# Performance work log

Hardware: AMD Instinct MI355X
Metric: run time of the kernel (lower is better)

Reference implementation:

```python
import jax, jax.numpy as jnp
import numpy as np
import math

Q, WAY, SHOT, M, D = 50, 5, 5, 196, 640
N_ITERS = 5
VAR_FLOOR = 0.01

def _inv_softplus(v):
    return math.log(math.expm1(v))

def setup_inputs() -> dict:
    key = jax.random.key(0)
    k1, k2, k3 = jax.random.split(key, 3)
    # L2-normalized tokens so cost = 1 - cosine sim is well-scaled
    q = jax.random.normal(k1, (Q, M, D), dtype=jnp.float32)
    q = q / jnp.linalg.norm(q, axis=-1, keepdims=True)
    s = jax.random.normal(k2, (WAY, SHOT, M, D), dtype=jnp.float32)
    s = s / jnp.linalg.norm(s, axis=-1, keepdims=True)
    var = jax.random.uniform(k3, (WAY, D), dtype=jnp.float32, minval=0.5, maxval=1.5)
    eps_raw = jnp.asarray(_inv_softplus(0.1), dtype=jnp.float32)           # eps_init=0.1
    tau_local_raw = jnp.asarray(_inv_softplus(1.0 - 0.01), dtype=jnp.float32)  # tau_local_init=1.0
    return {"query_tokens": q, "support_tokens": s, "variance": var,
            "eps_raw": eps_raw, "tau_local_raw": tau_local_raw}

def reference(query_tokens, support_tokens, variance, eps_raw, tau_local_raw):
    eps = jax.nn.softplus(eps_raw) + 1e-4
    tau = jax.nn.softplus(tau_local_raw) + 0.01
    way, shot, m, d = support_tokens.shape
    km = shot * m
    nq = query_tokens.shape[0]
    # dimension weights from variance (use_vhat_coupling=True)
    w = 1.0 / (variance + VAR_FLOOR)                              # [way, d]
    w = w / jnp.maximum(w.sum(axis=-1, keepdims=True), 1e-6) * d
    support_weighted = support_tokens.reshape(way, km, d) * w[:, None, :]
    sim = jnp.einsum('qmd,wkd->qwmk', query_tokens, support_weighted)  # [q, way, m, km]
    cost = 1.0 - sim
    log_K = -cost / eps
    log_mu = jnp.full((nq, way, m), -math.log(float(m)), dtype=log_K.dtype)
    log_nu = jnp.full((nq, way, km), -math.log(float(km)), dtype=log_K.dtype)

    def step(carry, _):
        u, v = carry
        v = log_nu - jax.nn.logsumexp(log_K + u[..., None], axis=-2)
        u = log_mu - jax.nn.logsumexp(log_K + v[..., None, :], axis=-1)
        return (u, v), None

    (u, v), _ = jax.lax.scan(step, (jnp.zeros_like(log_mu), jnp.zeros_like(log_nu)),
                             None, length=N_ITERS)
    gamma = jnp.exp(log_K + u[..., None] + v[..., None, :])
    ot_cost = jnp.sum(gamma * cost, axis=(-1, -2))                # [q, way]
    return -ot_cost / tau
```

## Files before the change

kernel.cpp:

```cpp
#include <hip/hip_runtime.h>
#include <hip/hip_bf16.h>
#include <hip/hip_fp16.h>

#define QN    50
#define NWAY  5
#define NPAIR 250
#define MM    196
#define KMM   980
#define DD    640
#define NITER 5

typedef __attribute__((ext_vector_type(8)))  short short8;
typedef __attribute__((ext_vector_type(16))) float f32x16;

#define EXP2F(x) __builtin_exp2f(x)
#define LOG2F(x) __builtin_log2f(x)
#define RCPF(x)  __builtin_amdgcn_rcpf(x)

__device__ __forceinline__ short bf16bits(float f) {
  __hip_bfloat16 h = __float2bfloat16(f);
  return *reinterpret_cast<short*>(&h);
}

__device__ __forceinline__ void h2AtomicAdd(__half2* addr, float a, float b) {
  unsigned int* ui = reinterpret_cast<unsigned int*>(addr);
  unsigned int old = __hip_atomic_load(ui, __ATOMIC_RELAXED, __HIP_MEMORY_SCOPE_AGENT);
  unsigned int assumed;
  do {
    assumed = old;
    __half2 cur = *reinterpret_cast<__half2*>(&assumed);
    float2 cf = __half22float2(cur);
    __half2 sum = __floats2half2_rn(cf.x + a, cf.y + b);
    unsigned int ns = *reinterpret_cast<unsigned int*>(&sum);
    old = atomicCAS(ui, assumed, ns);
  } while (old != assumed);
}

__global__ __launch_bounds__(256, 3)
void gemm_kernel(const float* __restrict__ qt, const float* __restrict__ st,
                 const float* __restrict__ var, const float* __restrict__ epsr,
                 __half* __restrict__ cost, __half* __restrict__ T1)
{
  __shared__ __align__(16) unsigned short Ash[128 * 64];
  __shared__ __align__(16) unsigned short Bsh[128 * 64];
  __shared__ __align__(16) float w_lds[DD];
  __shared__ float cs_lds[128];
  __shared__ float red_s;

  const int tid  = threadIdx.x;
  const int wv   = tid >> 6;
  const int lane = tid & 63;
  const int l31  = lane & 31;
  const int lh   = lane >> 5;
  const int wm   = wv >> 1;
  const int wn   = wv & 1;

  const int lg   = (blockIdx.x & 7) * 500 + (blockIdx.x >> 3);
  const int pair = lg >> 4;
  const int mt_  = (lg >> 3) & 1;
  const int nt_  = lg & 7;
  const int qi = pair / NWAY, wi = pair % NWAY;
  const int m0 = mt_ * 128, n0 = nt_ * 128;

  const float eps = logf(1.0f + expf(epsr[0])) + 1e-4f;
  const float C2  = 1.4426950408889634f / eps;

  float psum = 0.f;
  for (int d = tid; d < DD; d += 256) {
    float inv = 1.0f / (var[wi * DD + d] + 0.01f);
    w_lds[d] = inv; psum += inv;
  }
  #pragma unroll
  for (int s = 32; s; s >>= 1) psum += __shfl_xor(psum, s);
  if (tid == 0) red_s = 0.f;
  if (tid < 128) cs_lds[tid] = 0.f;
  __syncthreads();
  if (lane == 0) atomicAdd(&red_s, psum);
  __syncthreads();
  const float wsc = (float)DD / fmaxf(red_s, 1e-6f);
  for (int d = tid; d < DD; d += 256) w_lds[d] *= wsc;
  __syncthreads();

  const float* qb = qt + (size_t)qi * MM * DD;
  const float* sb = st + (size_t)wi * KMM * DD;

  f32x16 acc[2][2];
  #pragma unroll
  for (int i = 0; i < 2; ++i)
    #pragma unroll
    for (int j = 0; j < 2; ++j)
      #pragma unroll
      for (int e = 0; e < 16; ++e) acc[i][j][e] = 0.f;

  const int srow = tid >> 3;
  const int sslt = tid & 7;

  float4 ra0[4], ra1[4], rb0[4], rb1[4];

  #pragma unroll
  for (int i = 0; i < 4; ++i) {
    const int r = i * 32 + srow;
    const float* sa = qb + (size_t)min(m0 + r, MM - 1) * DD + sslt * 8;
    ra0[i] = *reinterpret_cast<const float4*>(sa);
    ra1[i] = *reinterpret_cast<const float4*>(sa + 4);
    const float* sbp = sb + (size_t)min(n0 + r, KMM - 1) * DD + sslt * 8;
    rb0[i] = *reinterpret_cast<const float4*>(sbp);
    rb1[i] = *reinterpret_cast<const float4*>(sbp + 4);
  }

  #pragma unroll
  for (int ks = 0; ks < 10; ++ks) {
    const int kd = ks * 64 + sslt * 8;
    float4 w0 = *reinterpret_cast<const float4*>(w_lds + kd);
    float4 w1 = *reinterpret_cast<const float4*>(w_lds + kd + 4);
    #pragma unroll
    for (int i = 0; i < 4; ++i) {
      const int r = i * 32 + srow;
      const int wslt = (sslt ^ (r & 7)) * 8;
      short8 pk;
      pk[0] = bf16bits(ra0[i].x); pk[1] = bf16bits(ra0[i].y);
      pk[2] = bf16bits(ra0[i].z); pk[3] = bf16bits(ra0[i].w);
      pk[4] = bf16bits(ra1[i].x); pk[5] = bf16bits(ra1[i].y);
      pk[6] = bf16bits(ra1[i].z); pk[7] = bf16bits(ra1[i].w);
      *reinterpret_cast<short8*>(&Ash[r * 64 + wslt]) = pk;
      short8 qk;
      qk[0] = bf16bits(rb0[i].x * w0.x); qk[1] = bf16bits(rb0[i].y * w0.y);
      qk[2] = bf16bits(rb0[i].z * w0.z); qk[3] = bf16bits(rb0[i].w * w0.w);
      qk[4] = bf16bits(rb1[i].x * w1.x); qk[5] = bf16bits(rb1[i].y * w1.y);
      qk[6] = bf16bits(rb1[i].z * w1.z); qk[7] = bf16bits(rb1[i].w * w1.w);
      *reinterpret_cast<short8*>(&Bsh[r * 64 + wslt]) = qk;
    }
    __syncthreads();
    if (ks < 9) {
      const int kn = (ks + 1) * 64 + sslt * 8;
      #pragma unroll
      for (int i = 0; i < 4; ++i) {
        const int r = i * 32 + srow;
        const float* sa = qb + (size_t)min(m0 + r, MM - 1) * DD + kn;
        ra0[i] = *reinterpret_cast<const float4*>(sa);
        ra1[i] = *reinterpret_cast<const float4*>(sa + 4);
        const float* sbp = sb + (size_t)min(n0 + r, KMM - 1) * DD + kn;
        rb0[i] = *reinterpret_cast<const float4*>(sbp);
        rb1[i] = *reinterpret_cast<const float4*>(sbp + 4);
      }
    }
    #pragma unroll
    for (int kk = 0; kk < 4; ++kk) {
      const int ph = ((kk * 2 + lh) ^ (l31 & 7)) * 8;
      short8 a0 = *reinterpret_cast<short8*>(&Ash[(wm * 64      + l31) * 64 + ph]);
      short8 a1 = *reinterpret_cast<short8*>(&Ash[(wm * 64 + 32 + l31) * 64 + ph]);
      short8 b0 = *reinterpret_cast<short8*>(&Bsh[(wn * 64      + l31) * 64 + ph]);
      short8 b1 = *reinterpret_cast<short8*>(&Bsh[(wn * 64 + 32 + l31) * 64 + ph]);
      acc[0][0] = __builtin_amdgcn_mfma_f32_32x32x16_bf16(a0, b0, acc[0][0], 0, 0, 0);
      acc[0][1] = __builtin_amdgcn_mfma_f32_32x32x16_bf16(a0, b1, acc[0][1], 0, 0, 0);
      acc[1][0] = __builtin_amdgcn_mfma_f32_32x32x16_bf16(a1, b0, acc[1][0], 0, 0, 0);
      acc[1][1] = __builtin_amdgcn_mfma_f32_32x32x16_bf16(a1, b1, acc[1][1], 0, 0, 0);
    }
    __syncthreads();
  }

  __half* cb = cost + (size_t)pair * MM * KMM;
  #pragma unroll
  for (int nt = 0; nt < 2; ++nt) {
    const int ncol = n0 + wn * 64 + nt * 32 + l31;
    float part = 0.f;
    #pragma unroll
    for (int mt = 0; mt < 2; ++mt) {
      #pragma unroll
      for (int r = 0; r < 16; ++r) {
        const int mrow = m0 + wm * 64 + mt * 32 + (r & 3) + 8 * (r >> 2) + 4 * lh;
        if (mrow < MM && ncol < KMM) {
          const float val = (acc[mt][nt][r] - 1.0f) * C2;
          cb[(size_t)mrow * KMM + ncol] = __float2half(val);
          part += EXP2F(val);
        }
      }
    }
    atomicAdd(&cs_lds[wn * 64 + nt * 32 + l31], part);
  }
  __syncthreads();
  if (tid < 64) {
    const int c0 = n0 + 2 * tid;
    if (c0 < KMM)
      h2AtomicAdd(reinterpret_cast<__half2*>(T1 + (size_t)pair * KMM + c0),
                  cs_lds[2 * tid], cs_lds[2 * tid + 1]);
  }
}

template<bool FIN>
__global__ __launch_bounds__(256)
void sweep_kernel(const __half* __restrict__ cost, const __half* __restrict__ Tin,
                  __half* __restrict__ Tout, const float* __restrict__ epsr,
                  const float* __restrict__ taur, float* __restrict__ outp)
{
  __shared__ float part[4][1024];
  const int tid  = threadIdx.x;
  const int wave = tid >> 6;
  const int lane = tid & 63;
  const int pair   = blockIdx.x / 7;
  const int mchunk = blockIdx.x % 7;

  const __half* cb = cost + (size_t)pair * MM * KMM;
  const __half* tp = Tin  + (size_t)pair * KMM;

  float iT[16], acc[16], p[16];
  #pragma unroll
  for (int j = 0; j < 4; ++j) {
    const int k = 4 * lane + 256 * j;
    if (k < KMM) {
      uint2 raw = *reinterpret_cast<const uint2*>(tp + k);
      float2 t01 = __half22float2(*reinterpret_cast<const __half2*>(&raw.x));
      float2 t23 = __half22float2(*reinterpret_cast<const __half2*>(&raw.y));
      iT[4 * j + 0] = RCPF(980.0f * t01.x);
      iT[4 * j + 1] = RCPF(980.0f * t01.y);
      iT[4 * j + 2] = RCPF(980.0f * t23.x);
      iT[4 * j + 3] = RCPF(980.0f * t23.y);
    } else {
      iT[4 * j + 0] = 0.f; iT[4 * j + 1] = 0.f;
      iT[4 * j + 2] = 0.f; iT[4 * j + 3] = 0.f;
    }
  }
  #pragma unroll
  for (int e = 0; e < 16; ++e) acc[e] = 0.f;

  float scal = 0.f, rowacc = 0.f;
  if (FIN) {
    const float eps = logf(1.0f + expf(epsr[0])) + 1e-4f;
    const float C2  = 1.4426950408889634f / eps;
    const float tau = logf(1.0f + expf(taur[0])) + 0.01f;
    scal = 1.0f / (tau * C2);
  }

  #pragma unroll
  for (int r = 0; r < 7; ++r) {
    const int m = mchunk * 28 + wave * 7 + r;
    const __half* rp = cb + (size_t)m * KMM;
    float A = 0.f, Bv = 0.f;
    #pragma unroll
    for (int j = 0; j < 4; ++j) {
      const int k = 4 * lane + 256 * j;
      if (k < KMM) {
        uint2 raw = *reinterpret_cast<const uint2*>(rp + k);
        float2 c01 = __half22float2(*reinterpret_cast<const __half2*>(&raw.x));
        float2 c23 = __half22float2(*reinterpret_cast<const __half2*>(&raw.y));
        float p0 = EXP2F(c01.x), p1 = EXP2F(c01.y);
        float p2 = EXP2F(c23.x), p3 = EXP2F(c23.y);
        p[4 * j + 0] = p0; p[4 * j + 1] = p1;
        p[4 * j + 2] = p2; p[4 * j + 3] = p3;
        float e0 = p0 * iT[4 * j + 0], e1 = p1 * iT[4 * j + 1];
        float e2 = p2 * iT[4 * j + 2], e3 = p3 * iT[4 * j + 3];
        A += (e0 + e1) + (e2 + e3);
        if (FIN) Bv += e0 * c01.x + e1 * c01.y + e2 * c23.x + e3 * c23.y;
      } else {
        p[4 * j + 0] = 0.f; p[4 * j + 1] = 0.f;
        p[4 * j + 2] = 0.f; p[4 * j + 3] = 0.f;
      }
    }
    #pragma unroll
    for (int s = 32; s; s >>= 1) {
      A += __shfl_xor(A, s);
      if (FIN) Bv += __shfl_xor(Bv, s);
    }
    const float up = RCPF(196.0f * A);
    if (FIN) {
      rowacc += Bv * up;
    } else {
      #pragma unroll
      for (int e = 0; e < 16; ++e) acc[e] += p[e] * up;
    }
  }

  if (FIN) {
    if (lane == 0) atomicAdd(outp + pair, rowacc * scal);
  } else {
    #pragma unroll
    for (int j = 0; j < 4; ++j) {
      const int k = 4 * lane + 256 * j;
      part[wave][k + 0] = acc[4 * j + 0];
      part[wave][k + 1] = acc[4 * j + 1];
      part[wave][k + 2] = acc[4 * j + 2];
      part[wave][k + 3] = acc[4 * j + 3];
    }
    __syncthreads();
    __half* top = Tout + (size_t)pair * KMM;
    for (int c2 = tid; c2 < KMM / 2; c2 += 256) {
      const int c = 2 * c2;
      float s0 = part[0][c]     + part[1][c]     + part[2][c]     + part[3][c];
      float s1 = part[0][c + 1] + part[1][c + 1] + part[2][c + 1] + part[3][c + 1];
      h2AtomicAdd(reinterpret_cast<__half2*>(top + c), s0, s1);
    }
  }
}

extern "C" void kernel_launch(void* const* d_in, const int* in_sizes, int n_in,
                              void* d_out, int out_size, void* d_ws, size_t ws_size,
                              hipStream_t stream) {
  const float* qt  = (const float*)d_in[0];
  const float* st  = (const float*)d_in[1];
  const float* var = (const float*)d_in[2];
  const float* er  = (const float*)d_in[3];
  const float* tr  = (const float*)d_in[4];
  float* out = (float*)d_out;

  char* ws = (char*)d_ws;
  __half* cost = (__half*)ws;
  __half* Ta   = (__half*)(ws + 96040000);
  __half* Tb   = (__half*)(ws + 96040000 + 490000);

  (void)hipMemsetAsync(out, 0, NPAIR * sizeof(float), stream);
  (void)hipMemsetAsync(Ta, 0, (size_t)NPAIR * KMM * sizeof(__half), stream);

  gemm_kernel<<<NPAIR * 16, 256, 0, stream>>>(qt, st, var, er, cost, Ta);

  __half* cur = Ta;
  __half* nxt = Tb;
  for (int it = 0; it < NITER - 1; ++it) {
    (void)hipMemsetAsync(nxt, 0, (size_t)NPAIR * KMM * sizeof(__half), stream);
    sweep_kernel<false><<<NPAIR * 7, 256, 0, stream>>>(cost, cur, nxt, er, tr, out);
    __half* t = cur; cur = nxt; nxt = t;
  }
  sweep_kernel<true><<<NPAIR * 7, 256, 0, stream>>>(cost, cur, nullptr, er, tr, out);
}
```

Measured before the change: 439.8 us.

## Store Sinkhorn log-kernel as FP8 E4M3 to halve cost-matrix traffic

The cost/log-kernel matrix is stored as software-encoded FP8 E4M3 bytes with a padded row stride of 984 instead of FP16. The constant -1 shift is dropped from the stored value and subtracted analytically in the final cost sum. The aim is to halve the bandwidth-bound traffic of the five sweep passes over the roughly 48 MB matrix. Pairs are also reordered way-major so blocks sharing a support set run close together, and the output index is remapped to match. The trade-off is much coarser quantization of the exponent argument (3 mantissa bits), which risks accuracy, plus extra ALU work to encode and decode.

```diff
diff --git a/kernel.cpp b/kernel.cpp
--- a/kernel.cpp
+++ b/kernel.cpp
@@ -7,6 +7,7 @@
 #define NPAIR 250
 #define MM    196
 #define KMM   980
+#define KP    984
 #define DD    640
 #define NITER 5
 
@@ -14,12 +15,30 @@
 typedef __attribute__((ext_vector_type(16))) float f32x16;
 
 #define EXP2F(x) __builtin_exp2f(x)
-#define LOG2F(x) __builtin_log2f(x)
 #define RCPF(x)  __builtin_amdgcn_rcpf(x)
+
+#define E4M3_UP 1.3292279957849159e36f
+#define E4M3_DN 7.5231638452626401e-37f
 
 __device__ __forceinline__ short bf16bits(float f) {
   __hip_bfloat16 h = __float2bfloat16(f);
   return *reinterpret_cast<short*>(&h);
+}
+
+__device__ __forceinline__ unsigned int f32_to_e4m3(float x) {
+  unsigned int b = __float_as_uint(x);
+  unsigned int sgn = (b >> 24) & 0x80u;
+  float a = __uint_as_float(b & 0x7FFFFFFFu);
+  a = fminf(a, 448.0f);
+  unsigned int z = __float_as_uint(a * E4M3_DN);
+  unsigned int mag = (z + 0x00080000u) >> 20;
+  return sgn | mag;
+}
+__device__ __forceinline__ float e4m3_to_f32(unsigned int v) {
+  return __uint_as_float(((v & 0x80u) << 24) | ((v & 0x7Fu) << 20)) * E4M3_UP;
+}
+__device__ __forceinline__ float dec8(unsigned int word, int byte) {
+  return e4m3_to_f32((word >> (8 * byte)) & 0xFFu);
 }
 
 __device__ __forceinline__ void h2AtomicAdd(__half2* addr, float a, float b) {
@@ -39,7 +58,7 @@
 __global__ __launch_bounds__(256, 3)
 void gemm_kernel(const float* __restrict__ qt, const float* __restrict__ st,
                  const float* __restrict__ var, const float* __restrict__ epsr,
-                 __half* __restrict__ cost, __half* __restrict__ T1)
+                 unsigned char* __restrict__ cost, __half* __restrict__ T1)
 {
   __shared__ __align__(16) unsigned short Ash[128 * 64];
   __shared__ __align__(16) unsigned short Bsh[128 * 64];
@@ -59,7 +78,7 @@
   const int pair = lg >> 4;
   const int mt_  = (lg >> 3) & 1;
   const int nt_  = lg & 7;
-  const int qi = pair / NWAY, wi = pair % NWAY;
+  const int wi = pair / 50, qi = pair % 50;
   const int m0 = mt_ * 128, n0 = nt_ * 128;
 
   const float eps = logf(1.0f + expf(epsr[0])) + 1e-4f;
@@ -96,7 +115,6 @@
   const int sslt = tid & 7;
 
   float4 ra0[4], ra1[4], rb0[4], rb1[4];
-
   #pragma unroll
   for (int i = 0; i < 4; ++i) {
     const int r = i * 32 + srow;
@@ -159,7 +177,7 @@
     __syncthreads();
   }
 
-  __half* cb = cost + (size_t)pair * MM * KMM;
+  unsigned char* cb = cost + (size_t)pair * (MM * KP);
   #pragma unroll
   for (int nt = 0; nt < 2; ++nt) {
     const int ncol = n0 + wn * 64 + nt * 32 + l31;
@@ -170,9 +188,9 @@
       for (int r = 0; r < 16; ++r) {
         const int mrow = m0 + wm * 64 + mt * 32 + (r & 3) + 8 * (r >> 2) + 4 * lh;
         if (mrow < MM && ncol < KMM) {
-          const float val = (acc[mt][nt][r] - 1.0f) * C2;
-          cb[(size_t)mrow * KMM + ncol] = __float2half(val);
-          part += EXP2F(val);
+          unsigned int enc = f32_to_e4m3(acc[mt][nt][r] * C2);
+          cb[(size_t)mrow * KP + ncol] = (unsigned char)enc;
+          part += EXP2F(e4m3_to_f32(enc));
         }
       }
     }
@@ -189,7 +207,7 @@
 
 template<bool FIN>
 __global__ __launch_bounds__(256)
-void sweep_kernel(const __half* __restrict__ cost, const __half* __restrict__ Tin,
+void sweep_kernel(const unsigned char* __restrict__ cost, const __half* __restrict__ Tin,
                   __half* __restrict__ Tout, const float* __restrict__ epsr,
                   const float* __restrict__ taur, float* __restrict__ outp)
 {
@@ -200,61 +218,70 @@
   const int pair   = blockIdx.x / 7;
   const int mchunk = blockIdx.x % 7;
 
-  const __half* cb = cost + (size_t)pair * MM * KMM;
-  const __half* tp = Tin  + (size_t)pair * KMM;
-
-  float iT[16], acc[16], p[16];
-  #pragma unroll
-  for (int j = 0; j < 4; ++j) {
-    const int k = 4 * lane + 256 * j;
-    if (k < KMM) {
-      uint2 raw = *reinterpret_cast<const uint2*>(tp + k);
-      float2 t01 = __half22float2(*reinterpret_cast<const __half2*>(&raw.x));
-      float2 t23 = __half22float2(*reinterpret_cast<const __half2*>(&raw.y));
-      iT[4 * j + 0] = RCPF(980.0f * t01.x);
-      iT[4 * j + 1] = RCPF(980.0f * t01.y);
-      iT[4 * j + 2] = RCPF(980.0f * t23.x);
-      iT[4 * j + 3] = RCPF(980.0f * t23.y);
-    } else {
-      iT[4 * j + 0] = 0.f; iT[4 * j + 1] = 0.f;
-      iT[4 * j + 2] = 0.f; iT[4 * j + 3] = 0.f;
-    }
-  }
+  const unsigned char* cb = cost + (size_t)pair * (MM * KP);
+  const __half* tp = Tin + (size_t)pair * KMM;
+
+  const int k1 = 8 * lane;
+  const int k2 = 512 + 8 * lane;
+
+  float iT[16];
+  {
+    uint2 ta = *reinterpret_cast<const uint2*>(tp + k1);
+    uint2 tb = *reinterpret_cast<const uint2*>(tp + k1 + 4);
+    uint2 tc = *reinterpret_cast<const uint2*>(tp + k2);
+    uint2 td = *reinterpret_cast<const uint2*>(tp + k2 + 4);
+    float2 f;
+    f = __half22float2(*reinterpret_cast<const __half2*>(&ta.x)); iT[0] = RCPF(980.f * f.x); iT[1] = RCPF(980.f * f.y);
+    f = __half22float2(*reinterpret_cast<const __half2*>(&ta.y)); iT[2] = RCPF(980.f * f.x); iT[3] = RCPF(980.f * f.y);
+    f = __half22float2(*reinterpret_cast<const __half2*>(&tb.x)); iT[4] = RCPF(980.f * f.x); iT[5] = RCPF(980.f * f.y);
+    f = __half22float2(*reinterpret_cast<const __half2*>(&tb.y)); iT[6] = RCPF(980.f * f.x); iT[7] = RCPF(980.f * f.y);
+    f = __half22float2(*reinterpret_cast<const __half2*>(&tc.x)); iT[8] = RCPF(980.f * f.x); iT[9] = RCPF(980.f * f.y);
+    f = __half22float2(*reinterpret_cast<const __half2*>(&tc.y)); iT[10] = RCPF(980.f * f.x); iT[11] = RCPF(980.f * f.y);
+    f = __half22float2(*reinterpret_cast<const __half2*>(&td.x)); iT[12] = RCPF(980.f * f.x); iT[13] = RCPF(980.f * f.y);
+    f = __half22float2(*reinterpret_cast<const __half2*>(&td.y)); iT[14] = RCPF(980.f * f.x); iT[15] = RCPF(980.f * f.y);
+    #pragma unroll
+    for (int e = 8; e < 16; ++e)
+      if (k2 + (e - 8) >= KMM) iT[e] = 0.f;
+  }
+
+  float acc[16];
   #pragma unroll
   for (int e = 0; e < 16; ++e) acc[e] = 0.f;
 
-  float scal = 0.f, rowacc = 0.f;
+  float scal = 0.f, c2f = 0.f, rowtot = 0.f;
   if (FIN) {
     const float eps = logf(1.0f + expf(epsr[0])) + 1e-4f;
-    const float C2  = 1.4426950408889634f / eps;
+    c2f = 1.4426950408889634f / eps;
     const float tau = logf(1.0f + expf(taur[0])) + 0.01f;
-    scal = 1.0f / (tau * C2);
+    scal = 1.0f / (tau * c2f);
   }
 
   #pragma unroll
   for (int r = 0; r < 7; ++r) {
     const int m = mchunk * 28 + wave * 7 + r;
-    const __half* rp = cb + (size_t)m * KMM;
+    const unsigned char* rp = cb + (size_t)m * KP;
+    uint2 w1 = *reinterpret_cast<const uint2*>(rp + k1);
+    uint2 w2 = *reinterpret_cast<const uint2*>(rp + k2);
+    float r_[16], p_[16];
+    #pragma unroll
+    for (int e = 0; e < 4; ++e) {
+      r_[e]      = dec8(w1.x, e);
+      r_[4 + e]  = dec8(w1.y, e);
+      r_[8 + e]  = dec8(w2.x, e);
+      r_[12 + e] = dec8(w2.y, e);
+    }
+    #pragma unroll
+    for (int e = 0; e < 16; ++e) p_[e] = EXP2F(r_[e]);
+    #pragma unroll
+    for (int e = 8; e < 16; ++e)
+      if (k2 + (e - 8) >= KMM) p_[e] = 0.f;
+
     float A = 0.f, Bv = 0.f;
     #pragma unroll
-    for (int j = 0; j < 4; ++j) {
-      const int k = 4 * lane + 256 * j;
-      if (k < KMM) {
-        uint2 raw = *reinterpret_cast<const uint2*>(rp + k);
-        float2 c01 = __half22float2(*reinterpret_cast<const __half2*>(&raw.x));
-        float2 c23 = __half22float2(*reinterpret_cast<const __half2*>(&raw.y));
-        float p0 = EXP2F(c01.x), p1 = EXP2F(c01.y);
-        float p2 = EXP2F(c23.x), p3 = EXP2F(c23.y);
-        p[4 * j + 0] = p0; p[4 * j + 1] = p1;
-        p[4 * j + 2] = p2; p[4 * j + 3] = p3;
-        float e0 = p0 * iT[4 * j + 0], e1 = p1 * iT[4 * j + 1];
-        float e2 = p2 * iT[4 * j + 2], e3 = p3 * iT[4 * j + 3];
-        A += (e0 + e1) + (e2 + e3);
-        if (FIN) Bv += e0 * c01.x + e1 * c01.y + e2 * c23.x + e3 * c23.y;
-      } else {
-        p[4 * j + 0] = 0.f; p[4 * j + 1] = 0.f;
-        p[4 * j + 2] = 0.f; p[4 * j + 3] = 0.f;
-      }
+    for (int e = 0; e < 16; ++e) {
+      float ee = p_[e] * iT[e];
+      A += ee;
+      if (FIN) Bv += ee * r_[e];
     }
     #pragma unroll
     for (int s = 32; s; s >>= 1) {
@@ -263,28 +290,27 @@
     }
     const float up = RCPF(196.0f * A);
     if (FIN) {
-      rowacc += Bv * up;
+      rowtot += Bv * up - c2f * (1.0f / 196.0f);
     } else {
       #pragma unroll
-      for (int e = 0; e < 16; ++e) acc[e] += p[e] * up;
+      for (int e = 0; e < 16; ++e) acc[e] += p_[e] * up;
     }
   }
 
   if (FIN) {
-    if (lane == 0) atomicAdd(outp + pair, rowacc * scal);
+    if (lane == 0) {
+      const int opair = (pair % 50) * NWAY + (pair / 50);
+      atomicAdd(outp + opair, rowtot * scal);
+    }
   } else {
     #pragma unroll
-    for (int j = 0; j < 4; ++j) {
-      const int k = 4 * lane + 256 * j;
-      part[wave][k + 0] = acc[4 * j + 0];
-      part[wave][k + 1] = acc[4 * j + 1];
-      part[wave][k + 2] = acc[4 * j + 2];
-      part[wave][k + 3] = acc[4 * j + 3];
-    }
+    for (int e = 0; e < 8; ++e) part[wave][k1 + e] = acc[e];
+    #pragma unroll
+    for (int e = 0; e < 8; ++e) part[wave][k2 + e] = acc[8 + e];
     __syncthreads();
     __half* top = Tout + (size_t)pair * KMM;
-    for (int c2 = tid; c2 < KMM / 2; c2 += 256) {
-      const int c = 2 * c2;
+    for (int c2c = tid; c2c < KMM / 2; c2c += 256) {
+      const int c = 2 * c2c;
       float s0 = part[0][c]     + part[1][c]     + part[2][c]     + part[3][c];
       float s1 = part[0][c + 1] + part[1][c + 1] + part[2][c + 1] + part[3][c + 1];
       h2AtomicAdd(reinterpret_cast<__half2*>(top + c), s0, s1);
@@ -303,9 +329,9 @@
   float* out = (float*)d_out;
 
   char* ws = (char*)d_ws;
-  __half* cost = (__half*)ws;
-  __half* Ta   = (__half*)(ws + 96040000);
-  __half* Tb   = (__half*)(ws + 96040000 + 490000);
+  unsigned char* cost = (unsigned char*)ws;
+  __half* Ta = (__half*)(ws + 48216000);
+  __half* Tb = (__half*)(ws + 48216000 + 490000);
 
   (void)hipMemsetAsync(out, 0, NPAIR * sizeof(float), stream);
   (void)hipMemsetAsync(Ta, 0, (size_t)NPAIR * KMM * sizeof(__half), stream);
```

Result: faster. 392.1 us (-10.8%).
